# Performance work log

Measured on AMD Instinct MI355X. Metric: run time of the kernel, lower is better.

## Reference

```python
import jax, jax.numpy as jnp
import numpy as np

B, S, D = 8, 2048, 1024
H = 4
K = D // 2          # expand_k = 0.5 -> key dim 512
V = D               # expand_v = 1.0 -> value dim 1024
DK, DV = K // H, V // H   # 128, 256
LOW_RANK = 16
GATE_LOGIT_NORM = 16.0
EPS = 1e-5
MLP_H = 4 * D


def _layernorm(x, g, b):
    mu = jnp.mean(x, axis=-1, keepdims=True)
    var = jnp.mean(jnp.square(x - mu), axis=-1, keepdims=True)
    return (x - mu) * jax.lax.rsqrt(var + EPS) * g + b


def _rmsnorm(x, w):
    ms = jnp.mean(jnp.square(x), axis=-1, keepdims=True)
    return x * jax.lax.rsqrt(ms + EPS) * w


def _gla(xn, Wq, Wk, Wv, Wg, Wgk1, Wgk2, bgk, gnorm_w, Wo):
    # projections ([B,S,D] @ [D,*]); weights stored as [in, out]
    q = (xn @ Wq).reshape(B, S, H, DK) * (DK ** -0.5)
    k = (xn @ Wk).reshape(B, S, H, DK)
    v = (xn @ Wv).reshape(B, S, H, DV)
    gk = jax.nn.log_sigmoid(xn @ Wgk1 @ Wgk2 + bgk) / GATE_LOGIT_NORM
    gk = gk.reshape(B, S, H, DK)

    def step(state, inp):
        qt, kt, vt, gt = inp                     # [B,H,DK], [B,H,DK], [B,H,DV], [B,H,DK]
        state = jnp.exp(gt)[..., None] * state + kt[..., None] * vt[..., None, :]
        ot = jnp.einsum('bhk,bhkv->bhv', qt, state)
        return state, ot

    init = jnp.zeros((B, H, DK, DV), xn.dtype)
    xs = (q.transpose(1, 0, 2, 3), k.transpose(1, 0, 2, 3),
          v.transpose(1, 0, 2, 3), gk.transpose(1, 0, 2, 3))
    _, o = jax.lax.scan(step, init, xs)          # o: [S,B,H,DV]
    o = o.transpose(1, 0, 2, 3)                  # [B,S,H,DV]

    g = (xn @ Wg).reshape(B, S, H, DV)
    o = _rmsnorm(o, gnorm_w) * g * jax.nn.sigmoid(g)   # RMSNorm + swish output gate
    return o.reshape(B, S, V) @ Wo


def setup_inputs() -> dict:
    key = jax.random.key(0)
    ks = jax.random.split(key, 16)
    sd = 0.02
    return {
        'x': jax.random.normal(ks[0], (B, S, D), jnp.float32),
        'ln1_g': jnp.ones((D,), jnp.float32),
        'ln1_b': jnp.zeros((D,), jnp.float32),
        'Wq': jax.random.normal(ks[1], (D, K), jnp.float32) * sd,
        'Wk': jax.random.normal(ks[2], (D, K), jnp.float32) * sd,
        'Wv': jax.random.normal(ks[3], (D, V), jnp.float32) * sd,
        'Wg': jax.random.normal(ks[4], (D, V), jnp.float32) * sd,
        'Wgk1': jax.random.normal(ks[5], (D, LOW_RANK), jnp.float32) * sd,
        'Wgk2': jax.random.normal(ks[6], (LOW_RANK, K), jnp.float32) * sd,
        'bgk': jnp.zeros((K,), jnp.float32),
        'gnorm_w': jnp.ones((DV,), jnp.float32),
        'Wo': jax.random.normal(ks[7], (V, D), jnp.float32) * sd,
        'ln2_g': jnp.ones((D,), jnp.float32),
        'ln2_b': jnp.zeros((D,), jnp.float32),
        'W1': jax.random.normal(ks[8], (D, MLP_H), jnp.float32) * sd,
        'b1': jnp.zeros((MLP_H,), jnp.float32),
        'W2': jax.random.normal(ks[9], (MLP_H, D), jnp.float32) * sd,
        'b2': jnp.zeros((D,), jnp.float32),
    }


def reference(x, ln1_g, ln1_b, Wq, Wk, Wv, Wg, Wgk1, Wgk2, bgk, gnorm_w, Wo,
              ln2_g, ln2_b, W1, b1, W2, b2):
    # pre-norm GLA block, eval mode (dropout = identity)
    attn_out = _gla(_layernorm(x, ln1_g, ln1_b), Wq, Wk, Wv, Wg, Wgk1, Wgk2, bgk, gnorm_w, Wo)
    x = x + attn_out
    h = _layernorm(x, ln2_g, ln2_b)
    h = jax.nn.gelu(h @ W1 + b1, approximate=False) @ W2 + b2
    return x + h
```

## Files before the change

kernel.cpp:

```cpp
#include <hip/hip_runtime.h>
#include <stdint.h>


typedef unsigned short u16t;
typedef __attribute__((ext_vector_type(8))) short bf16x8;
typedef __attribute__((ext_vector_type(4))) float f32x4;
typedef __attribute__((ext_vector_type(4))) unsigned short u16x4;

__device__ __forceinline__ float bf2f(unsigned short u){ union{unsigned int i; float f;} v; v.i=((unsigned int)u)<<16; return v.f; }
__device__ __forceinline__ unsigned short f2bf(float f){ union{unsigned int i; float f;} v; v.f=f; unsigned int r=v.i+0x7FFFu+((v.i>>16)&1u); return (unsigned short)(r>>16); }
__device__ __forceinline__ f32x4 cvt4(u16x4 u){ f32x4 r; r[0]=bf2f(u[0]); r[1]=bf2f(u[1]); r[2]=bf2f(u[2]); r[3]=bf2f(u[3]); return r; }

__device__ __forceinline__ float gelu_f(float t){
  const float t3 = t*t*t;
  const float y = 2.3021183f*t + 0.10295465f*t3;
  const float e = __builtin_amdgcn_exp2f(y);
  return t - t*__builtin_amdgcn_rcpf(e + 1.f);
}

__device__ __forceinline__ void gload_lds16(const unsigned short* g, unsigned short* l)
{
  __builtin_amdgcn_global_load_lds(
      (const __attribute__((address_space(1))) unsigned int*)g,
      (__attribute__((address_space(3))) unsigned int*)l,
      16, 0, 0);
}

__global__ void k_transpose_multi(const float* __restrict__ Wq, const float* __restrict__ Wk,
                                  const float* __restrict__ Wv, const float* __restrict__ Wg,
                                  const float* __restrict__ Wo, const float* __restrict__ W1,
                                  const float* __restrict__ W2,
                                  unsigned short* __restrict__ WPT, unsigned short* __restrict__ WOT,
                                  unsigned short* __restrict__ W1T, unsigned short* __restrict__ W2T)
{
  __shared__ float tile[32][33];
  int bid = blockIdx.x;
  const float* src; unsigned short* dst; int Kin, N, nx;
  if      (bid < 512)  { src=Wq; dst=WPT;                          Kin=1024; N=512;  nx=16;  }
  else if (bid < 1024) { src=Wk; dst=WPT+(size_t)512*1024;         Kin=1024; N=512;  nx=16;  bid-=512;  }
  else if (bid < 2048) { src=Wv; dst=WPT+(size_t)1024*1024;        Kin=1024; N=1024; nx=32;  bid-=1024; }
  else if (bid < 3072) { src=Wg; dst=WPT+(size_t)2048*1024;        Kin=1024; N=1024; nx=32;  bid-=2048; }
  else if (bid < 4096) { src=Wo; dst=WOT;                          Kin=1024; N=1024; nx=32;  bid-=3072; }
  else if (bid < 8192) { src=W1; dst=W1T;                          Kin=1024; N=4096; nx=128; bid-=4096; }
  else                 { src=W2; dst=W2T;                          Kin=4096; N=1024; nx=32;  bid-=8192; }
  const int n0 = (bid % nx)*32, k0 = (bid / nx)*32;
  const int tx = threadIdx.x, ty = threadIdx.y;
  #pragma unroll
  for (int i = 0; i < 4; ++i)
    tile[ty + i*8][tx] = src[(size_t)(k0 + ty + i*8)*N + n0 + tx];
  __syncthreads();
  #pragma unroll
  for (int i = 0; i < 4; ++i)
    dst[(size_t)(n0 + ty + i*8)*Kin + k0 + tx] = f2bf(tile[tx][ty + i*8]);
}

__global__ void k_wgk(const float* __restrict__ Wgk1, const float* __restrict__ Wgk2, unsigned short* __restrict__ dstT)
{
  const int idx = blockIdx.x*256 + threadIdx.x;
  const int i = idx & 1023, j = idx >> 10;
  float s = 0.f;
  #pragma unroll
  for (int r = 0; r < 16; ++r) s += Wgk1[i*16 + r] * Wgk2[r*512 + j];
  dstT[(size_t)j*1024 + i] = f2bf(s);
}

__global__ void k_vtrans(const unsigned short* __restrict__ proj, const unsigned short* __restrict__ kt,
                         unsigned short* __restrict__ vtg, unsigned short* __restrict__ ktt)
{
  __shared__ unsigned short tile[32][33];
  const int tt = blockIdx.x, zz = blockIdx.y, bh = blockIdx.z;
  const int b = bh >> 2, h = bh & 3;
  const int tx = threadIdx.x, ty = threadIdx.y;
  if (zz < 8) {
    const int dvt = zz;
    #pragma unroll
    for (int i = 0; i < 4; ++i)
      tile[ty + i*8][tx] = proj[((size_t)b*2048 + tt*32 + ty + i*8)*3584 + 1024 + h*256 + dvt*32 + tx];
    __syncthreads();
    #pragma unroll
    for (int i = 0; i < 4; ++i)
      vtg[((size_t)bh*256 + dvt*32 + ty + i*8)*2048 + tt*32 + tx] = tile[tx][ty + i*8];
  } else {
    const int dkt = zz - 8;
    #pragma unroll
    for (int i = 0; i < 4; ++i)
      tile[ty + i*8][tx] = kt[((size_t)bh*2048 + tt*32 + ty + i*8)*128 + dkt*32 + tx];
    __syncthreads();
    #pragma unroll
    for (int i = 0; i < 4; ++i)
      ktt[((size_t)bh*128 + dkt*32 + ty + i*8)*2048 + tt*32 + tx] = tile[tx][ty + i*8];
  }
}

__global__ __launch_bounds__(256) void k_layernorm(const float* __restrict__ x, const float* __restrict__ g,
                                                   const float* __restrict__ b, unsigned short* __restrict__ out)
{
  const int row = blockIdx.x, tid = threadIdx.x;
  const float4 xv = *(const float4*)&x[(size_t)row*1024 + tid*4];
  float s  = xv.x + xv.y + xv.z + xv.w;
  float sq = xv.x*xv.x + xv.y*xv.y + xv.z*xv.z + xv.w*xv.w;
  #pragma unroll
  for (int o = 32; o > 0; o >>= 1) { s += __shfl_xor(s, o); sq += __shfl_xor(sq, o); }
  __shared__ float red[8];
  const int w = tid >> 6;
  if ((tid & 63) == 0) { red[w] = s; red[4 + w] = sq; }
  __syncthreads();
  s  = red[0] + red[1] + red[2] + red[3];
  sq = red[4] + red[5] + red[6] + red[7];
  const float mu = s * (1.f/1024.f);
  const float var = sq * (1.f/1024.f) - mu*mu;
  const float rs = rsqrtf(var + 1e-5f);
  float xe[4] = {xv.x, xv.y, xv.z, xv.w};
  u16x4 o4;
  #pragma unroll
  for (int i = 0; i < 4; ++i) {
    const int c = tid*4 + i;
    o4[i] = f2bf((xe[i] - mu) * rs * g[c] + b[c]);
  }
  *(u16x4*)&out[(size_t)row*1024 + tid*4] = o4;
}

template<int EPI>
__global__ __launch_bounds__(512, 2)
void gemm256(const unsigned short* __restrict__ A, const unsigned short* __restrict__ Bt,
             int N, int K,
             float* outF, unsigned short* outH,
             const float* resid, const float* bias)
{
  __shared__ __align__(16) unsigned short lds[65536];
  const int tid = threadIdx.x;
  const int lane = tid & 63, w = tid >> 6;
  const int wr = w >> 2, wc = w & 3;
  const int l15 = lane & 15, lq = lane >> 4;

  const int nwg = gridDim.x * gridDim.y;
  const int bid = blockIdx.y * gridDim.x + blockIdx.x;
  const int q = nwg >> 3, r = nwg & 7;
  const int xcd = bid & 7, lid = bid >> 3;
  const int sw = (xcd < r ? xcd*(q+1) : r*(q+1) + (xcd - r)*q) + lid;
  const int row0 = (sw / gridDim.x) * 256;
  const int col0 = (sw % gridDim.x) * 256;

  const int rA_ = tid >> 3;
  const int cswz = 8 * ((tid & 7) ^ (rA_ & 7));
  const unsigned short* baseA[2][2];
  const unsigned short* baseB[2][2];
  #pragma unroll
  for (int h = 0; h < 2; ++h)
    #pragma unroll
    for (int L = 0; L < 2; ++L) {
      baseA[h][L] = A  + (size_t)(row0 + h*128 + L*64 + rA_) * K + cswz;
      baseB[h][L] = Bt + (size_t)(col0 + h*128 + L*64 + rA_) * K + cswz;
    }

  const int NT = K >> 6;
  const int NI = NT >> 1;

  f32x4 acc[8][4];
  #pragma unroll
  for (int m = 0; m < 8; ++m)
    #pragma unroll
    for (int n = 0; n < 4; ++n) { acc[m][n][0]=0.f; acc[m][n][1]=0.f; acc[m][n][2]=0.f; acc[m][n][3]=0.f; }

  bf16x8 af[4][2];
  bf16x8 bfr[2][2][2];

  #define STAGE(CH, T)                                                         \
    {                                                                          \
      const int tt = ((T) < NT) ? (T) : (T) - 2;                               \
      const int dbase = (tt & 1) * 32768 + (CH) * 8192;                        \
      const int ktt2 = tt << 6;                                                \
      _Pragma("unroll")                                                        \
      for (int L = 0; L < 2; ++L) {                                            \
        const unsigned short* gp =                                             \
            ((CH) < 2 ? baseA[(CH) & 1][L] : baseB[(CH) & 1][L]) + ktt2;       \
        gload_lds16(gp, (unsigned short*)&lds[dbase + L*4096 + w*512]);        \
      }                                                                        \
    }

  #define DS_A(CB)                                                             \
    { _Pragma("unroll")                                                        \
      for (int mm = 0; mm < 4; ++mm) {                                         \
        const int rl = wr*64 + mm*16 + l15;                                    \
        const int co = (l15 & 7) * 8;                                          \
        af[mm][0] = *(const bf16x8*)&lds[(CB) + rl*64 + ((lq*8) ^ co)];        \
        af[mm][1] = *(const bf16x8*)&lds[(CB) + rl*64 + ((32 + lq*8) ^ co)];   \
      } }

  #define DS_B(CB, QN)                                                         \
    { _Pragma("unroll")                                                        \
      for (int nn = 0; nn < 2; ++nn) {                                         \
        const int rl = wc*32 + nn*16 + l15;                                    \
        const int co = (l15 & 7) * 8;                                          \
        bfr[QN][nn][0] = *(const bf16x8*)&lds[(CB) + (2+(QN))*8192 + rl*64 + ((lq*8) ^ co)];      \
        bfr[QN][nn][1] = *(const bf16x8*)&lds[(CB) + (2+(QN))*8192 + rl*64 + ((32 + lq*8) ^ co)]; \
      } }

  #define PRE_MFMA()                                                           \
    { __builtin_amdgcn_s_barrier();                                            \
      asm volatile("s_waitcnt lgkmcnt(0)" ::: "memory");                       \
      __builtin_amdgcn_sched_barrier(0); }

  #define MMA(QM, QN)                                                          \
    { __builtin_amdgcn_s_setprio(1);                                           \
      _Pragma("unroll")                                                        \
      for (int mm = 0; mm < 4; ++mm)                                           \
        _Pragma("unroll")                                                      \
        for (int nn = 0; nn < 2; ++nn) {                                       \
          acc[(QM)*4+mm][(QN)*2+nn] = __builtin_amdgcn_mfma_f32_16x16x32_bf16( \
              af[mm][0], bfr[QN][nn][0], acc[(QM)*4+mm][(QN)*2+nn], 0, 0, 0);  \
          acc[(QM)*4+mm][(QN)*2+nn] = __builtin_amdgcn_mfma_f32_16x16x32_bf16( \
              af[mm][1], bfr[QN][nn][1], acc[(QM)*4+mm][(QN)*2+nn], 0, 0, 0);  \
        }                                                                      \
      __builtin_amdgcn_s_setprio(0); }

  #define POSTW(VN)                                                            \
    { asm volatile("s_waitcnt vmcnt(" #VN ")" ::: "memory");                   \
      __builtin_amdgcn_sched_barrier(0);                                       \
      __builtin_amdgcn_s_barrier(); }

  #define POSTN() { __builtin_amdgcn_s_barrier(); }

  STAGE(0, 0); STAGE(2, 0); STAGE(1, 0); STAGE(3, 0); STAGE(0, 1); STAGE(2, 1);
  asm volatile("s_waitcnt vmcnt(4)" ::: "memory");
  __builtin_amdgcn_sched_barrier(0);
  __builtin_amdgcn_s_barrier();

  for (int i = 0; i < NI; ++i) {
    const int t0 = 2*i, t1 = 2*i + 1;
    DS_A(0); DS_B(0, 0); STAGE(1, t1);
    PRE_MFMA(); MMA(0, 0); POSTN();
    DS_B(0, 1); STAGE(3, t1);
    PRE_MFMA(); MMA(0, 1); POSTN();
    DS_A(8192); STAGE(0, t0 + 2);
    PRE_MFMA(); MMA(1, 0); POSTN();
    STAGE(2, t0 + 2);
    PRE_MFMA(); MMA(1, 1); POSTW(4);
    DS_A(32768); DS_B(32768, 0); STAGE(1, t0 + 2);
    PRE_MFMA(); MMA(0, 0); POSTN();
    DS_B(32768, 1); STAGE(3, t0 + 2);
    PRE_MFMA(); MMA(0, 1); POSTN();
    DS_A(32768 + 8192); STAGE(0, t1 + 2);
    PRE_MFMA(); MMA(1, 0); POSTN();
    STAGE(2, t1 + 2);
    PRE_MFMA(); MMA(1, 1); POSTW(4);
  }
  #undef STAGE
  #undef DS_A
  #undef DS_B
  #undef PRE_MFMA
  #undef MMA
  #undef POSTW
  #undef POSTN

  #pragma unroll
  for (int qm = 0; qm < 2; ++qm)
    #pragma unroll
    for (int mm = 0; mm < 4; ++mm)
      #pragma unroll
      for (int qn = 0; qn < 2; ++qn)
        #pragma unroll
        for (int nn = 0; nn < 2; ++nn)
          #pragma unroll
          for (int ii = 0; ii < 4; ++ii) {
            const int rr = row0 + qm*128 + wr*64 + mm*16 + lq*4 + ii;
            const int cc = col0 + qn*128 + wc*32 + nn*16 + l15;
            const size_t idx = (size_t)rr * N + cc;
            const float v = acc[qm*4+mm][qn*2+nn][ii];
            if constexpr (EPI == 0) {
              outH[idx] = f2bf(v);
            } else if constexpr (EPI == 1) {
              outF[idx] = v + resid[idx];
            } else if constexpr (EPI == 2) {
              outH[idx] = f2bf(gelu_f(v + bias[cc]));
            } else {
              outF[idx] = v + bias[cc] + resid[idx];
            }
          }
}

__global__ __launch_bounds__(128) void k_scanprep(const unsigned short* __restrict__ proj, const float* __restrict__ bgk,
                                                  unsigned short* __restrict__ qt, unsigned short* __restrict__ kt,
                                                  float* __restrict__ eac)
{
  const int c = blockIdx.x & 31, bh = blockIdx.x >> 5;
  const int b = bh >> 2, h = bh & 3;
  const int dk = threadIdx.x;
  const size_t tok0 = (size_t)b*2048 + c*64;
  const float bg = bgk[h*128 + dk];
  float A = 0.f, ea = 1.f;
  for (int t = 0; t < 64; ++t) {
    const size_t prow = (tok0 + t) * 3584;
    const float qv = bf2f(proj[prow + h*128 + dk]);
    const float kv = bf2f(proj[prow + 512 + h*128 + dk]);
    const float z = bf2f(proj[prow + 3072 + h*128 + dk]) + bg;
    const float az = fabsf(z);
    const float sp = fmaxf(-z, 0.f)
                   + 0.69314718f*__builtin_amdgcn_logf(1.f + __builtin_amdgcn_exp2f(-1.44269504f*az));
    A -= sp * 0.0625f;
    ea = __builtin_amdgcn_exp2f(A * 1.44269504f);
    const float em = __builtin_amdgcn_rcpf(ea);
    const size_t orow = ((size_t)bh*2048 + c*64 + t)*128 + dk;
    qt[orow] = f2bf(qv * ea * 0.08838834764831845f);
    kt[orow] = f2bf(kv * em);
  }
  eac[((size_t)bh*32 + c)*128 + dk] = ea;
}

__global__ __launch_bounds__(512) void k_seqstate(const unsigned short* __restrict__ ktt,
                                                  const unsigned short* __restrict__ vtg,
                                                  const float* __restrict__ eac,
                                                  unsigned short* __restrict__ sst)
{
  __shared__ __align__(16) unsigned short SLq[16384];
  const int bid = blockIdx.x;
  const int bh = bid >> 3, dks = (bid >> 2) & 1, dvs = bid & 3;
  const int tid = threadIdx.x, lane = tid & 63, w = tid >> 6;
  const int wr = w >> 2, wc = w & 3;
  const int l15 = lane & 15, lq = lane >> 4;
  const int kc8 = (lane & 7) * 8;

  #define SSTAGE(C, BUF)                                                        \
    { { const int o = w*512 + lane*8;                                           \
        const int dkl = o >> 6;                                                 \
        gload_lds16(&ktt[((size_t)bh*128 + dks*64 + dkl)*2048 + (C)*64 + (kc8 ^ ((dkl & 7) << 3))], \
                    (unsigned short*)&SLq[(BUF)*8192 + w*512]); }                \
      { const int o = w*512 + lane*8;                                           \
        const int dvl = o >> 6;                                                 \
        gload_lds16(&vtg[((size_t)bh*256 + dvs*64 + dvl)*2048 + (C)*64 + (kc8 ^ ((dvl & 7) << 3))], \
                    (unsigned short*)&SLq[(BUF)*8192 + 4096 + w*512]); } }

  f32x4 acc[2];
  acc[0][0]=0.f; acc[0][1]=0.f; acc[0][2]=0.f; acc[0][3]=0.f;
  acc[1] = acc[0];

  SSTAGE(0, 0);
  asm volatile("s_waitcnt vmcnt(0)" ::: "memory");
  __builtin_amdgcn_sched_barrier(0);
  __builtin_amdgcn_s_barrier();

  for (int c = 0; c < 32; ++c) {
    const int buf = c & 1;
    if (c + 1 < 32) {
      SSTAGE(c + 1, buf ^ 1);
      asm volatile("s_waitcnt vmcnt(2)" ::: "memory");
    } else {
      asm volatile("s_waitcnt vmcnt(0)" ::: "memory");
    }
    __builtin_amdgcn_sched_barrier(0);
    __builtin_amdgcn_s_barrier();

    const size_t srow = (((size_t)bh*32 + c)*256 + dvs*64 + wc*16 + l15)*128;
    #pragma unroll
    for (int mm = 0; mm < 2; ++mm) {
      u16x4 tj;
      tj[0]=f2bf(acc[mm][0]); tj[1]=f2bf(acc[mm][1]); tj[2]=f2bf(acc[mm][2]); tj[3]=f2bf(acc[mm][3]);
      *(u16x4*)&sst[srow + dks*64 + wr*32 + mm*16 + lq*4] = tj;
    }
    f32x4 ev[2];
    #pragma unroll
    for (int mm = 0; mm < 2; ++mm)
      ev[mm] = *(const f32x4*)&eac[(size_t)(bh*32 + c)*128 + dks*64 + wr*32 + mm*16 + lq*4];

    const int base = buf*8192;
    bf16x8 afr[2][2], bfrg[2];
    #pragma unroll
    for (int mm = 0; mm < 2; ++mm) {
      const int rl = wr*32 + mm*16 + l15;
      const int co = (rl & 7) << 3;
      afr[mm][0] = *(const bf16x8*)&SLq[base + rl*64 + ((lq*8) ^ co)];
      afr[mm][1] = *(const bf16x8*)&SLq[base + rl*64 + ((32 + lq*8) ^ co)];
    }
    {
      const int dvl = wc*16 + l15;
      const int co = (dvl & 7) << 3;
      bfrg[0] = *(const bf16x8*)&SLq[base + 4096 + dvl*64 + ((lq*8) ^ co)];
      bfrg[1] = *(const bf16x8*)&SLq[base + 4096 + dvl*64 + ((32 + lq*8) ^ co)];
    }
    asm volatile("s_waitcnt lgkmcnt(0)" ::: "memory");
    __builtin_amdgcn_sched_barrier(0);
    #pragma unroll
    for (int k4 = 0; k4 < 2; ++k4)
      #pragma unroll
      for (int mm = 0; mm < 2; ++mm)
        acc[mm] = __builtin_amdgcn_mfma_f32_16x16x32_bf16(afr[mm][k4], bfrg[k4], acc[mm], 0, 0, 0);
    #pragma unroll
    for (int mm = 0; mm < 2; ++mm)
      #pragma unroll
      for (int i = 0; i < 4; ++i)
        acc[mm][i] *= ev[mm][i];
    __builtin_amdgcn_s_barrier();
  }
  #undef SSTAGE
}

__global__ __launch_bounds__(512) void k_attn_out(const unsigned short* __restrict__ qt,
                                                  const unsigned short* __restrict__ kt,
                                                  const unsigned short* __restrict__ vtg,
                                                  const unsigned short* __restrict__ sst,
                                                  const unsigned short* __restrict__ proj,
                                                  const float* __restrict__ gnw,
                                                  unsigned short* __restrict__ og)
{
  __shared__ __align__(16) unsigned short SL[61440];
  __shared__ float ssq[64];
  const int c = blockIdx.x & 31, bh = blockIdx.x >> 5;
  const int b = bh >> 2, h = bh & 3;
  const int tid = threadIdx.x, lane = tid & 63, w = tid >> 6;
  const int wr = w >> 2, wc = w & 3;
  const int l15 = lane & 15, lq = lane >> 4;
  const size_t qk0 = (size_t)bh*2048 + c*64;
  const size_t tok0 = (size_t)b*2048 + c*64;
  const int key15 = (l15 & 7) << 3;

  if (tid < 64) ssq[tid] = 0.f;

  const int kc8 = (lane & 7) * 8;
  #pragma unroll
  for (int it = 0; it < 2; ++it) {
    const int o = it*4096 + w*512 + lane*8;
    const int ch = o >> 12, r = (o >> 6) & 63;
    gload_lds16(&kt[(qk0 + r)*128 + ch*64 + (kc8 ^ ((r & 7) << 3))],
                (unsigned short*)&SL[53248 + it*4096 + w*512]);
  }
  #pragma unroll
  for (int it = 0; it < 4; ++it) {
    const int o = it*4096 + w*512 + lane*8;
    const int dv = o >> 6;
    gload_lds16(&vtg[((size_t)bh*256 + dv)*2048 + c*64 + (kc8 ^ ((dv & 7) << 3))],
                (unsigned short*)&SL[4096 + it*4096 + w*512]);
  }
  #pragma unroll
  for (int it = 0; it < 8; ++it) {
    const int o = it*4096 + w*512 + lane*8;
    const int ch = o >> 14, dv = (o >> 6) & 255;
    gload_lds16(&sst[((size_t)(bh*32 + c)*256 + dv)*128 + ch*64 + (kc8 ^ ((dv & 7) << 3))],
                (unsigned short*)&SL[20480 + it*4096 + w*512]);
  }
  bf16x8 aq[2][4];
  #pragma unroll
  for (int mm = 0; mm < 2; ++mm)
    #pragma unroll
    for (int k4 = 0; k4 < 4; ++k4)
      aq[mm][k4] = *(const bf16x8*)&qt[(qk0 + wr*32 + mm*16 + l15)*128 + k4*32 + lq*8];

  __syncthreads();

  f32x4 accp[2];
  accp[0][0]=0.f; accp[0][1]=0.f; accp[0][2]=0.f; accp[0][3]=0.f;
  accp[1] = accp[0];
  #pragma unroll
  for (int k4 = 0; k4 < 4; ++k4) {
    const int ch = k4 >> 1, k0c = (k4 & 1) * 32;
    const bf16x8 bk = *(const bf16x8*)&SL[53248 + ch*4096 + (wc*16 + l15)*64 + ((k0c + lq*8) ^ key15)];
    accp[0] = __builtin_amdgcn_mfma_f32_16x16x32_bf16(aq[0][k4], bk, accp[0], 0, 0, 0);
    accp[1] = __builtin_amdgcn_mfma_f32_16x16x32_bf16(aq[1][k4], bk, accp[1], 0, 0, 0);
  }
  #pragma unroll
  for (int mm = 0; mm < 2; ++mm)
    #pragma unroll
    for (int i = 0; i < 4; ++i) {
      const int rg = wr*32 + mm*16 + lq*4 + i;
      const int cg = wc*16 + l15;
      SL[rg*64 + (cg ^ ((rg & 7) << 3))] = f2bf((cg <= rg) ? accp[mm][i] : 0.f);
    }
  __syncthreads();

  f32x4 acco[2][4];
  #pragma unroll
  for (int mm = 0; mm < 2; ++mm)
    #pragma unroll
    for (int nn = 0; nn < 4; ++nn) { acco[mm][nn][0]=0.f; acco[mm][nn][1]=0.f; acco[mm][nn][2]=0.f; acco[mm][nn][3]=0.f; }

  #pragma unroll
  for (int t4 = 0; t4 < 2; ++t4) {
    bf16x8 ap[2];
    #pragma unroll
    for (int mm = 0; mm < 2; ++mm) {
      const int r = wr*32 + mm*16 + l15;
      ap[mm] = *(const bf16x8*)&SL[r*64 + ((t4*32 + lq*8) ^ key15)];
    }
    #pragma unroll
    for (int nn = 0; nn < 4; ++nn) {
      const int dv = wc*64 + nn*16 + l15;
      const bf16x8 bv = *(const bf16x8*)&SL[4096 + dv*64 + ((t4*32 + lq*8) ^ key15)];
      acco[0][nn] = __builtin_amdgcn_mfma_f32_16x16x32_bf16(ap[0], bv, acco[0][nn], 0, 0, 0);
      acco[1][nn] = __builtin_amdgcn_mfma_f32_16x16x32_bf16(ap[1], bv, acco[1][nn], 0, 0, 0);
    }
  }
  #pragma unroll
  for (int k4 = 0; k4 < 4; ++k4) {
    const int ch = k4 >> 1, k0c = (k4 & 1) * 32;
    #pragma unroll
    for (int nn = 0; nn < 4; ++nn) {
      const int dv = wc*64 + nn*16 + l15;
      const bf16x8 bs = *(const bf16x8*)&SL[20480 + ch*16384 + dv*64 + ((k0c + lq*8) ^ key15)];
      acco[0][nn] = __builtin_amdgcn_mfma_f32_16x16x32_bf16(aq[0][k4], bs, acco[0][nn], 0, 0, 0);
      acco[1][nn] = __builtin_amdgcn_mfma_f32_16x16x32_bf16(aq[1][k4], bs, acco[1][nn], 0, 0, 0);
    }
  }

  #pragma unroll
  for (int mm = 0; mm < 2; ++mm) {
    float part[4];
    #pragma unroll
    for (int i = 0; i < 4; ++i) {
      float s = 0.f;
      #pragma unroll
      for (int nn = 0; nn < 4; ++nn) s += acco[mm][nn][i]*acco[mm][nn][i];
      s += __shfl_xor(s, 1); s += __shfl_xor(s, 2); s += __shfl_xor(s, 4); s += __shfl_xor(s, 8);
      part[i] = s;
    }
    if (l15 == 0) {
      #pragma unroll
      for (int i = 0; i < 4; ++i)
        atomicAdd(&ssq[wr*32 + mm*16 + lq*4 + i], part[i]);
    }
  }
  __syncthreads();

  #pragma unroll
  for (int mm = 0; mm < 2; ++mm)
    #pragma unroll
    for (int i = 0; i < 4; ++i) {
      const int rg = wr*32 + mm*16 + lq*4 + i;
      const float rs = rsqrtf(ssq[rg] * (1.f/256.f) + 1e-5f);
      const size_t token = tok0 + rg;
      #pragma unroll
      for (int nn = 0; nn < 4; ++nn) {
        const int dv = wc*64 + nn*16 + l15;
        const float gf = bf2f(proj[token*3584 + 2048 + h*256 + dv]);
        const float swv = gf * __builtin_amdgcn_rcpf(1.f + __builtin_amdgcn_exp2f(-1.44269504f*gf));
        og[token*1024 + h*256 + dv] = f2bf(acco[mm][nn][i] * rs * gnw[dv] * swv);
      }
    }
}

extern "C" void kernel_launch(void* const* d_in, const int* in_sizes, int n_in,
                              void* d_out, int out_size, void* d_ws, size_t ws_size,
                              hipStream_t stream)
{
  (void)in_sizes; (void)n_in; (void)out_size; (void)ws_size;
  const float* x    = (const float*)d_in[0];
  const float* ln1g = (const float*)d_in[1];
  const float* ln1b = (const float*)d_in[2];
  const float* Wq   = (const float*)d_in[3];
  const float* Wk   = (const float*)d_in[4];
  const float* Wv   = (const float*)d_in[5];
  const float* Wg   = (const float*)d_in[6];
  const float* Wgk1 = (const float*)d_in[7];
  const float* Wgk2 = (const float*)d_in[8];
  const float* bgk  = (const float*)d_in[9];
  const float* gnw  = (const float*)d_in[10];
  const float* Wo   = (const float*)d_in[11];
  const float* ln2g = (const float*)d_in[12];
  const float* ln2b = (const float*)d_in[13];
  const float* W1   = (const float*)d_in[14];
  const float* b1   = (const float*)d_in[15];
  const float* W2   = (const float*)d_in[16];
  const float* b2   = (const float*)d_in[17];
  float* out = (float*)d_out;
  char* ws = (char*)d_ws;

  u16t*  XN   = (u16t*)(ws + 0);
  u16t*  KTT  = (u16t*)(ws + 0);
  u16t*  OG   = (u16t*)(ws + 0);
  u16t*  WPT  = (u16t*)(ws + 33554432);
  u16t*  WOT  = (u16t*)(ws + 40894464);
  u16t*  W1T  = (u16t*)(ws + 42991616);
  u16t*  W2T  = (u16t*)(ws + 51380224);
  u16t*  PROJ = (u16t*)(ws + 59768832);
  u16t*  QT   = (u16t*)(ws + 177209344);
  u16t*  KT   = (u16t*)(ws + 193986560);
  float* EAC  = (float*)(ws + 210763776);
  u16t*  VT   = (u16t*)(ws + 211288064);
  u16t*  H2   = (u16t*)(ws + 211288064);
  u16t*  HID  = PROJ;
  u16t*  SST  = (u16t*)d_out;

  k_transpose_multi<<<12288, dim3(32,8), 0, stream>>>(Wq, Wk, Wv, Wg, Wo, W1, W2, WPT, WOT, W1T, W2T);
  k_wgk<<<2048, 256, 0, stream>>>(Wgk1, Wgk2, WPT + (size_t)3072*1024);

  k_layernorm<<<16384, 256, 0, stream>>>(x, ln1g, ln1b, XN);
  gemm256<0><<<dim3(14,64), 512, 0, stream>>>(XN, WPT, 3584, 1024, nullptr, PROJ, nullptr, nullptr);
  k_scanprep<<<1024, 128, 0, stream>>>(PROJ, bgk, QT, KT, EAC);
  k_vtrans<<<dim3(64,12,32), dim3(32,8), 0, stream>>>(PROJ, KT, VT, KTT);
  k_seqstate<<<256, 512, 0, stream>>>(KTT, VT, EAC, SST);
  k_attn_out<<<1024, 512, 0, stream>>>(QT, KT, VT, SST, PROJ, gnw, OG);
  gemm256<1><<<dim3(4,64),  512, 0, stream>>>(OG, WOT, 1024, 1024, out, nullptr, x, nullptr);
  k_layernorm<<<16384, 256, 0, stream>>>(out, ln2g, ln2b, H2);
  gemm256<2><<<dim3(16,64), 512, 0, stream>>>(H2, W1T, 4096, 1024, nullptr, HID, nullptr, b1);
  gemm256<3><<<dim3(4,64),  512, 0, stream>>>(HID, W2T, 1024, 4096, out, nullptr, out, b2);
}
```

Before: 693.3 us.

## Switch GEMM to 16 waves with 64x64 per-wave tiles and simple double buffering

Rewrites the 256x256 bf16 GEMM to run 1024 threads per block instead of 512, so each wave computes a 64x64 sub-tile instead of 128x64. The hand-interleaved quarter-tile pipeline, with staggered staging and many barriers, is replaced by a plain double-buffered k-loop: stage the next tile, wait, barrier, then two MFMA halves. The aim is more waves to hide latency and fewer barriers per k-step. The cost is lower register-level reuse per wave and the loss of the fine-grained overlap of loads with MFMAs. LDS use per block is unchanged.

```diff
diff --git a/kernel.cpp b/kernel.cpp
--- a/kernel.cpp
+++ b/kernel.cpp
@@ -121,7 +121,7 @@
 }
 
 template<int EPI>
-__global__ __launch_bounds__(512, 2)
+__global__ __launch_bounds__(1024, 3)
 void gemm256(const unsigned short* __restrict__ A, const unsigned short* __restrict__ Bt,
              int N, int K,
              float* outF, unsigned short* outH,
@@ -143,140 +143,99 @@
 
   const int rA_ = tid >> 3;
   const int cswz = 8 * ((tid & 7) ^ (rA_ & 7));
-  const unsigned short* baseA[2][2];
-  const unsigned short* baseB[2][2];
-  #pragma unroll
-  for (int h = 0; h < 2; ++h)
-    #pragma unroll
-    for (int L = 0; L < 2; ++L) {
-      baseA[h][L] = A  + (size_t)(row0 + h*128 + L*64 + rA_) * K + cswz;
-      baseB[h][L] = Bt + (size_t)(col0 + h*128 + L*64 + rA_) * K + cswz;
-    }
+  const unsigned short* baseA[2];
+  const unsigned short* baseB[2];
+  #pragma unroll
+  for (int h = 0; h < 2; ++h) {
+    baseA[h] = A  + (size_t)(row0 + h*128 + rA_) * K + cswz;
+    baseB[h] = Bt + (size_t)(col0 + h*128 + rA_) * K + cswz;
+  }
 
   const int NT = K >> 6;
-  const int NI = NT >> 1;
-
-  f32x4 acc[8][4];
-  #pragma unroll
-  for (int m = 0; m < 8; ++m)
+
+  f32x4 acc[4][4];
+  #pragma unroll
+  for (int m = 0; m < 4; ++m)
     #pragma unroll
     for (int n = 0; n < 4; ++n) { acc[m][n][0]=0.f; acc[m][n][1]=0.f; acc[m][n][2]=0.f; acc[m][n][3]=0.f; }
 
-  bf16x8 af[4][2];
-  bf16x8 bfr[2][2][2];
-
-  #define STAGE(CH, T)                                                         \
+  const int carA = (wr >> 1) * 8192;
+  const int carB = 16384 + (wc >> 1) * 8192;
+  const int rowA = (wr & 1) * 64;
+  const int rowB = (wc & 1) * 64;
+  const int co = (l15 & 7) * 8;
+
+  #define STAGE4(T)                                                            \
     {                                                                          \
-      const int tt = ((T) < NT) ? (T) : (T) - 2;                               \
-      const int dbase = (tt & 1) * 32768 + (CH) * 8192;                        \
-      const int ktt2 = tt << 6;                                                \
+      const int dbase = ((T) & 1) * 32768;                                     \
+      const int ktt2 = (T) << 6;                                               \
+      gload_lds16(baseA[0] + ktt2, (unsigned short*)&lds[dbase +         w*512]); \
+      gload_lds16(baseA[1] + ktt2, (unsigned short*)&lds[dbase +  8192 + w*512]); \
+      gload_lds16(baseB[0] + ktt2, (unsigned short*)&lds[dbase + 16384 + w*512]); \
+      gload_lds16(baseB[1] + ktt2, (unsigned short*)&lds[dbase + 24576 + w*512]); \
+    }
+
+  #define MMAH(BUF, H)                                                         \
+    {                                                                          \
+      bf16x8 af[4], bfr[4];                                                    \
       _Pragma("unroll")                                                        \
-      for (int L = 0; L < 2; ++L) {                                            \
-        const unsigned short* gp =                                             \
-            ((CH) < 2 ? baseA[(CH) & 1][L] : baseB[(CH) & 1][L]) + ktt2;       \
-        gload_lds16(gp, (unsigned short*)&lds[dbase + L*4096 + w*512]);        \
-      }                                                                        \
-    }
-
-  #define DS_A(CB)                                                             \
-    { _Pragma("unroll")                                                        \
-      for (int mm = 0; mm < 4; ++mm) {                                         \
-        const int rl = wr*64 + mm*16 + l15;                                    \
-        const int co = (l15 & 7) * 8;                                          \
-        af[mm][0] = *(const bf16x8*)&lds[(CB) + rl*64 + ((lq*8) ^ co)];        \
-        af[mm][1] = *(const bf16x8*)&lds[(CB) + rl*64 + ((32 + lq*8) ^ co)];   \
-      } }
-
-  #define DS_B(CB, QN)                                                         \
-    { _Pragma("unroll")                                                        \
-      for (int nn = 0; nn < 2; ++nn) {                                         \
-        const int rl = wc*32 + nn*16 + l15;                                    \
-        const int co = (l15 & 7) * 8;                                          \
-        bfr[QN][nn][0] = *(const bf16x8*)&lds[(CB) + (2+(QN))*8192 + rl*64 + ((lq*8) ^ co)];      \
-        bfr[QN][nn][1] = *(const bf16x8*)&lds[(CB) + (2+(QN))*8192 + rl*64 + ((32 + lq*8) ^ co)]; \
-      } }
-
-  #define PRE_MFMA()                                                           \
-    { __builtin_amdgcn_s_barrier();                                            \
+      for (int mm = 0; mm < 4; ++mm)                                           \
+        af[mm] = *(const bf16x8*)&lds[(BUF) + carA + (rowA + mm*16 + l15)*64   \
+                                      + (((H)*32 + lq*8) ^ co)];               \
+      _Pragma("unroll")                                                        \
+      for (int nn = 0; nn < 4; ++nn)                                           \
+        bfr[nn] = *(const bf16x8*)&lds[(BUF) + carB + (rowB + nn*16 + l15)*64  \
+                                       + (((H)*32 + lq*8) ^ co)];              \
       asm volatile("s_waitcnt lgkmcnt(0)" ::: "memory");                       \
-      __builtin_amdgcn_sched_barrier(0); }
-
-  #define MMA(QM, QN)                                                          \
-    { __builtin_amdgcn_s_setprio(1);                                           \
+      __builtin_amdgcn_sched_barrier(0);                                       \
+      if (H) { __builtin_amdgcn_s_barrier(); }   \
+      __builtin_amdgcn_s_setprio(1);                                           \
       _Pragma("unroll")                                                        \
       for (int mm = 0; mm < 4; ++mm)                                           \
         _Pragma("unroll")                                                      \
-        for (int nn = 0; nn < 2; ++nn) {                                       \
-          acc[(QM)*4+mm][(QN)*2+nn] = __builtin_amdgcn_mfma_f32_16x16x32_bf16( \
-              af[mm][0], bfr[QN][nn][0], acc[(QM)*4+mm][(QN)*2+nn], 0, 0, 0);  \
-          acc[(QM)*4+mm][(QN)*2+nn] = __builtin_amdgcn_mfma_f32_16x16x32_bf16( \
-              af[mm][1], bfr[QN][nn][1], acc[(QM)*4+mm][(QN)*2+nn], 0, 0, 0);  \
-        }                                                                      \
-      __builtin_amdgcn_s_setprio(0); }
-
-  #define POSTW(VN)                                                            \
-    { asm volatile("s_waitcnt vmcnt(" #VN ")" ::: "memory");                   \
-      __builtin_amdgcn_sched_barrier(0);                                       \
-      __builtin_amdgcn_s_barrier(); }
-
-  #define POSTN() { __builtin_amdgcn_s_barrier(); }
-
-  STAGE(0, 0); STAGE(2, 0); STAGE(1, 0); STAGE(3, 0); STAGE(0, 1); STAGE(2, 1);
-  asm volatile("s_waitcnt vmcnt(4)" ::: "memory");
-  __builtin_amdgcn_sched_barrier(0);
-  __builtin_amdgcn_s_barrier();
-
-  for (int i = 0; i < NI; ++i) {
-    const int t0 = 2*i, t1 = 2*i + 1;
-    DS_A(0); DS_B(0, 0); STAGE(1, t1);
-    PRE_MFMA(); MMA(0, 0); POSTN();
-    DS_B(0, 1); STAGE(3, t1);
-    PRE_MFMA(); MMA(0, 1); POSTN();
-    DS_A(8192); STAGE(0, t0 + 2);
-    PRE_MFMA(); MMA(1, 0); POSTN();
-    STAGE(2, t0 + 2);
-    PRE_MFMA(); MMA(1, 1); POSTW(4);
-    DS_A(32768); DS_B(32768, 0); STAGE(1, t0 + 2);
-    PRE_MFMA(); MMA(0, 0); POSTN();
-    DS_B(32768, 1); STAGE(3, t0 + 2);
-    PRE_MFMA(); MMA(0, 1); POSTN();
-    DS_A(32768 + 8192); STAGE(0, t1 + 2);
-    PRE_MFMA(); MMA(1, 0); POSTN();
-    STAGE(2, t1 + 2);
-    PRE_MFMA(); MMA(1, 1); POSTW(4);
-  }
-  #undef STAGE
-  #undef DS_A
-  #undef DS_B
-  #undef PRE_MFMA
-  #undef MMA
-  #undef POSTW
-  #undef POSTN
-
-  #pragma unroll
-  for (int qm = 0; qm < 2; ++qm)
-    #pragma unroll
-    for (int mm = 0; mm < 4; ++mm)
+        for (int nn = 0; nn < 4; ++nn)                                         \
+          acc[mm][nn] = __builtin_amdgcn_mfma_f32_16x16x32_bf16(               \
+              af[mm], bfr[nn], acc[mm][nn], 0, 0, 0);                          \
+      __builtin_amdgcn_s_setprio(0);                                           \
+    }
+
+  STAGE4(0);
+  for (int t = 0; t < NT; ++t) {
+    const int buf = (t & 1) * 32768;
+    if (t + 1 < NT) {
+      STAGE4(t + 1);
+      asm volatile("s_waitcnt vmcnt(4)" ::: "memory");
+    } else {
+      asm volatile("s_waitcnt vmcnt(0)" ::: "memory");
+    }
+    __builtin_amdgcn_sched_barrier(0);
+    __builtin_amdgcn_s_barrier();
+    MMAH(buf, 0);
+    MMAH(buf, 1);
+  }
+  #undef STAGE4
+  #undef MMAH
+
+  #pragma unroll
+  for (int mm = 0; mm < 4; ++mm)
+    #pragma unroll
+    for (int nn = 0; nn < 4; ++nn)
       #pragma unroll
-      for (int qn = 0; qn < 2; ++qn)
-        #pragma unroll
-        for (int nn = 0; nn < 2; ++nn)
-          #pragma unroll
-          for (int ii = 0; ii < 4; ++ii) {
-            const int rr = row0 + qm*128 + wr*64 + mm*16 + lq*4 + ii;
-            const int cc = col0 + qn*128 + wc*32 + nn*16 + l15;
-            const size_t idx = (size_t)rr * N + cc;
-            const float v = acc[qm*4+mm][qn*2+nn][ii];
-            if constexpr (EPI == 0) {
-              outH[idx] = f2bf(v);
-            } else if constexpr (EPI == 1) {
-              outF[idx] = v + resid[idx];
-            } else if constexpr (EPI == 2) {
-              outH[idx] = f2bf(gelu_f(v + bias[cc]));
-            } else {
-              outF[idx] = v + bias[cc] + resid[idx];
-            }
-          }
+      for (int ii = 0; ii < 4; ++ii) {
+        const int rr = row0 + wr*64 + mm*16 + lq*4 + ii;
+        const int cc = col0 + wc*64 + nn*16 + l15;
+        const size_t idx = (size_t)rr * N + cc;
+        const float v = acc[mm][nn][ii];
+        if constexpr (EPI == 0) {
+          outH[idx] = f2bf(v);
+        } else if constexpr (EPI == 1) {
+          outF[idx] = v + resid[idx];
+        } else if constexpr (EPI == 2) {
+          outH[idx] = f2bf(gelu_f(v + bias[cc]));
+        } else {
+          outF[idx] = v + bias[cc] + resid[idx];
+        }
+      }
 }
 
 __global__ __launch_bounds__(128) void k_scanprep(const unsigned short* __restrict__ proj, const float* __restrict__ bgk,
@@ -582,13 +541,13 @@
   k_wgk<<<2048, 256, 0, stream>>>(Wgk1, Wgk2, WPT + (size_t)3072*1024);
 
   k_layernorm<<<16384, 256, 0, stream>>>(x, ln1g, ln1b, XN);
-  gemm256<0><<<dim3(14,64), 512, 0, stream>>>(XN, WPT, 3584, 1024, nullptr, PROJ, nullptr, nullptr);
+  gemm256<0><<<dim3(14,64), 1024, 0, stream>>>(XN, WPT, 3584, 1024, nullptr, PROJ, nullptr, nullptr);
   k_scanprep<<<1024, 128, 0, stream>>>(PROJ, bgk, QT, KT, EAC);
   k_vtrans<<<dim3(64,12,32), dim3(32,8), 0, stream>>>(PROJ, KT, VT, KTT);
   k_seqstate<<<256, 512, 0, stream>>>(KTT, VT, EAC, SST);
   k_attn_out<<<1024, 512, 0, stream>>>(QT, KT, VT, SST, PROJ, gnw, OG);
-  gemm256<1><<<dim3(4,64),  512, 0, stream>>>(OG, WOT, 1024, 1024, out, nullptr, x, nullptr);
+  gemm256<1><<<dim3(4,64),  1024, 0, stream>>>(OG, WOT, 1024, 1024, out, nullptr, x, nullptr);
   k_layernorm<<<16384, 256, 0, stream>>>(out, ln2g, ln2b, H2);
-  gemm256<2><<<dim3(16,64), 512, 0, stream>>>(H2, W1T, 4096, 1024, nullptr, HID, nullptr, b1);
-  gemm256<3><<<dim3(4,64),  512, 0, stream>>>(HID, W2T, 1024, 4096, out, nullptr, out, b2);
-}
+  gemm256<2><<<dim3(16,64), 1024, 0, stream>>>(H2, W1T, 4096, 1024, nullptr, HID, nullptr, b1);
+  gemm256<3><<<dim3(4,64),  1024, 0, stream>>>(HID, W2T, 1024, 4096, out, nullptr, out, b2);
+}
```

After: 672.4 us. 1.03x faster.
